# Performance work log

Hardware: AMD Instinct MI355X
Metric: run time of the kernel (lower is better)

The kernel has to match this reference:

```python
import jax, jax.numpy as jnp
import numpy as np

N = 100000   # nodes
E = 3200000  # edges (avg degree 32)
H = 75       # hidden
ITER = 3     # num_layers


def setup_inputs() -> dict:
    key = jax.random.key(0)
    ks = jax.random.split(key, 16)
    s = 0.1  # weight scale
    x = jax.random.normal(ks[0], (N, H), jnp.float32)
    src = jax.random.randint(ks[1], (E,), 0, N)
    dst = jax.random.randint(ks[2], (E,), 0, N)
    edge_index = jnp.stack([src, dst]).astype(jnp.int32)
    rn = lambda k, shp: jax.random.normal(k, shp, jnp.float32) * s
    return {
        "x": x,
        "edge_index": edge_index,
        "eps": jnp.zeros((1,), jnp.float32),      # GIN train_eps, init 0
        "w1": rn(ks[3], (H, H)), "b1": jnp.zeros((H,), jnp.float32),
        "w2": rn(ks[4], (H, H)), "b2": jnp.zeros((H,), jnp.float32),
        "w_ih": rn(ks[5], (3 * H, H)), "w_hh": rn(ks[6], (3 * H, H)),
        "b_ih": jnp.zeros((3 * H,), jnp.float32), "b_hh": jnp.zeros((3 * H,), jnp.float32),
        "wc1": rn(ks[7], (ITER * H, 2 * H)), "bc1": jnp.zeros((2 * H,), jnp.float32),
        "wc2": rn(ks[8], (2 * H, H)), "bc2": jnp.zeros((H,), jnp.float32),
    }


def reference(x, edge_index, eps, w1, b1, w2, b2, w_ih, w_hh, b_ih, b_hh, wc1, bc1, wc2, bc2):
    src, dst = edge_index[0], edge_index[1]

    def gin(xt):
        # sum aggregation over incoming edges (gather -> scatter-add)
        agg = jax.ops.segment_sum(xt[src], dst, num_segments=N)
        z = (1.0 + eps[0]) * xt + agg
        return jnp.maximum(z @ w1 + b1, 0.0) @ w2 + b2

    def gru_step(inp, h):
        # torch.nn.GRU single step; gate order: r, z, n
        gi = inp @ w_ih.T + b_ih
        gh = h @ w_hh.T + b_hh
        ir, iz, inn = jnp.split(gi, 3, axis=-1)
        hr, hz, hn = jnp.split(gh, 3, axis=-1)
        r = jax.nn.sigmoid(ir + hr)
        zg = jax.nn.sigmoid(iz + hz)
        n = jnp.tanh(inn + r * hn)
        return (1.0 - zg) * n + zg * h

    h = x   # h0 = x.unsqueeze(0)
    xt = x
    node_states = []
    for _ in range(ITER):
        m = jnp.maximum(gin(xt), 0.0)
        h = gru_step(m, h)
        xt = h  # GRU output == hidden state for single layer/step
        node_states.append(xt)

    cat = jnp.concatenate(node_states, axis=1)  # [N, ITER*H]
    readout = jnp.maximum(cat @ wc1 + bc1, 0.0) @ wc2 + bc2
    return (xt, readout)
```

## Files before the change

### kernel.cpp

```cpp
#include <hip/hip_runtime.h>

#define NN 100000
#define EE 3200000
#define N2 100032
#define NBUCK 782
#define CPAD 16
#define CHUNK 12288

typedef _Float16 f16;
typedef _Float16 f16x8 __attribute__((ext_vector_type(8)));
typedef float f32x4 __attribute__((ext_vector_type(4)));
typedef unsigned int u32;

#define MFMA(a, b, c) __builtin_amdgcn_mfma_f32_16x16x32_f16((a), (b), (c), 0, 0, 0)


__global__ __launch_bounds__(256) void bhist_kernel(const int4* __restrict__ dst4,
                                                    int* __restrict__ bcnt) {
  __shared__ int h[2][NBUCK];
  int tid = threadIdx.x;
  for (int i = tid; i < 2 * NBUCK; i += 256) ((int*)h)[i] = 0;
  __syncthreads();
  int r = (tid >> 7) & 1;
  for (int i = blockIdx.x * 256 + tid; i < EE / 4; i += gridDim.x * 256) {
    int4 d = dst4[i];
    atomicAdd(&h[r][d.x >> 7], 1);
    atomicAdd(&h[r][d.y >> 7], 1);
    atomicAdd(&h[r][d.z >> 7], 1);
    atomicAdd(&h[r][d.w >> 7], 1);
  }
  __syncthreads();
  for (int i = tid; i < NBUCK; i += 256) {
    int v = h[0][i] + h[1][i];
    if (v) atomicAdd(&bcnt[i * CPAD], v);
  }
}

__global__ __launch_bounds__(1024) void bscan_kernel(const int* __restrict__ bcnt,
                                                     int* __restrict__ bbase,
                                                     int* __restrict__ bcur,
                                                     int* __restrict__ rs) {
  __shared__ int sb[1024];
  int tid = threadIdx.x;
  int c = (tid < NBUCK) ? bcnt[tid * CPAD] : 0;
  int v = c;
  sb[tid] = v;
  __syncthreads();
  for (int off = 1; off < 1024; off <<= 1) {
    int t = (tid >= off) ? sb[tid - off] : 0;
    __syncthreads();
    v += t;
    sb[tid] = v;
    __syncthreads();
  }
  if (tid < NBUCK) {
    bbase[tid] = v - c;
    bcur[tid * CPAD] = v - c;
  }
  if (tid == 0) {
    bbase[NBUCK] = EE;
    rs[NN] = EE;
  }
}

__global__ __launch_bounds__(256) void binB_kernel(const int* __restrict__ src,
                                                   const int* __restrict__ dst,
                                                   int* __restrict__ bcur,
                                                   u32* __restrict__ ebuf) {
  __shared__ int hist[NBUCK];
  __shared__ int base[NBUCK];
  int tid = threadIdx.x;
  int e0 = blockIdx.x * CHUNK;
  int e1 = e0 + CHUNK;
  if (e1 > EE) e1 = EE;
  for (int i = tid; i < NBUCK; i += 256) hist[i] = 0;
  __syncthreads();
  for (int e = e0 + tid * 4; e < e1; e += 1024) {
    int4 d = *(const int4*)(dst + e);
    atomicAdd(&hist[d.x >> 7], 1);
    atomicAdd(&hist[d.y >> 7], 1);
    atomicAdd(&hist[d.z >> 7], 1);
    atomicAdd(&hist[d.w >> 7], 1);
  }
  __syncthreads();
  for (int i = tid; i < NBUCK; i += 256) {
    int c = hist[i];
    if (c) base[i] = atomicAdd(&bcur[i * CPAD], c);
  }
  __syncthreads();
  for (int i = tid; i < NBUCK; i += 256) hist[i] = 0;
  __syncthreads();
  for (int e = e0 + tid * 4; e < e1; e += 1024) {
    int4 d = *(const int4*)(dst + e);
    int4 s = *(const int4*)(src + e);
    int b, loc;
    b = d.x >> 7; loc = atomicAdd(&hist[b], 1);
    ebuf[base[b] + loc] = (u32)s.x | ((u32)(d.x & 127) << 17);
    b = d.y >> 7; loc = atomicAdd(&hist[b], 1);
    ebuf[base[b] + loc] = (u32)s.y | ((u32)(d.y & 127) << 17);
    b = d.z >> 7; loc = atomicAdd(&hist[b], 1);
    ebuf[base[b] + loc] = (u32)s.z | ((u32)(d.z & 127) << 17);
    b = d.w >> 7; loc = atomicAdd(&hist[b], 1);
    ebuf[base[b] + loc] = (u32)s.w | ((u32)(d.w & 127) << 17);
  }
}

__global__ __launch_bounds__(256) void binC_kernel(const u32* __restrict__ ebuf,
                                                   const int* __restrict__ bbase,
                                                   int* __restrict__ rs,
                                                   int* __restrict__ csr) {
  __shared__ int cnt[128], sc[128], cur[128];
  int b = blockIdx.x, tid = threadIdx.x;
  int e0 = bbase[b], e1 = bbase[b + 1];
  if (tid < 128) cnt[tid] = 0;
  __syncthreads();
  for (int e = e0 + tid; e < e1; e += 256) atomicAdd(&cnt[ebuf[e] >> 17], 1);
  __syncthreads();
  if (tid < 128) sc[tid] = cnt[tid];
  __syncthreads();
  for (int off = 1; off < 128; off <<= 1) {
    int t = 0;
    if (tid < 128 && tid >= off) t = sc[tid - off];
    __syncthreads();
    if (tid < 128) sc[tid] += t;
    __syncthreads();
  }
  if (tid < 128) {
    int gpos = e0 + sc[tid] - cnt[tid];
    int node = b * 128 + tid;
    if (node < NN) rs[node] = gpos;
    cur[tid] = gpos;
  }
  __syncthreads();
  for (int e = e0 + tid; e < e1; e += 256) {
    u32 p = ebuf[e];
    int pos = atomicAdd(&cur[p >> 17], 1);
    csr[pos] = (int)(p & 0x1FFFFu);
  }
}


__device__ __forceinline__ f16 pack_one(const float* __restrict__ W,
                                        const float* __restrict__ bias, int rel, int K, int Nc,
                                        int KG, int trans, int bslot) {
  int e = rel & 7, nn = (rel >> 3) & 15;
  int g = (rel >> 7) % KG, nb = (rel >> 7) / KG;
  int k = g * 8 + e, n = nb * 16 + nn;
  float v = 0.f;
  if (n < Nc) {
    if (k < K) v = trans ? W[n * K + k] : W[k * Nc + n];
    else if (k == bslot) v = bias[n];
  }
  return (f16)v;
}

__global__ __launch_bounds__(256) void packall_kernel(const float* __restrict__ w1,
                                                      const float* __restrict__ b1,
                                                      const float* __restrict__ w2,
                                                      const float* __restrict__ b2,
                                                      const float* __restrict__ wih,
                                                      const float* __restrict__ bih,
                                                      const float* __restrict__ whh,
                                                      const float* __restrict__ bhh,
                                                      const float* __restrict__ wc1,
                                                      const float* __restrict__ bc1,
                                                      const float* __restrict__ wc2,
                                                      const float* __restrict__ bc2,
                                                      f16* __restrict__ wp) {
  int i = blockIdx.x * 256 + threadIdx.x;
  if (i >= 120320) return;
  f16 v;
  if (i < 7680) v = pack_one(w1, b1, i, 75, 75, 12, 0, 95);
  else if (i < 15360) v = pack_one(w2, b2, i - 7680, 75, 75, 12, 0, 95);
  else if (i < 38400) {
    int r = i - 15360, g = r / 7680;
    v = pack_one(wih + g * 5625, bih + g * 75, r - g * 7680, 75, 75, 12, 1, 95);
  } else if (i < 61440) {
    int r = i - 38400, g = r / 7680;
    v = pack_one(whh + g * 5625, bhh + g * 75, r - g * 7680, 75, 75, 12, 1, 95);
  } else if (i < 107520) {
    int rel = i - 61440;
    int e = rel & 7, nn = (rel >> 3) & 15;
    int g = (rel >> 7) % 36, nb = (rel >> 7) / 36;
    int q = g * 8 + e, buf = q / 96, kk = q - buf * 96, n = nb * 16 + nn;
    float f = 0.f;
    if (n < 150) {
      if (kk < 75) f = wc1[(buf * 75 + kk) * 150 + n];
      else if (kk == 95 && buf == 0) f = bc1[n];
    }
    v = (f16)f;
  } else v = pack_one(wc2, bc2, i - 107520, 150, 75, 20, 0, 159);
  wp[i] = v;
}


__global__ __launch_bounds__(256) void convx_kernel(const float* __restrict__ x,
                                                    f16* __restrict__ xp) {
  int i = blockIdx.x * 256 + threadIdx.x;
  if (i >= N2 * 96) return;
  int r = i / 96, c = i - r * 96;
  float v = (r < NN && c < 75) ? x[r * 75 + c] : (c == 95 ? 1.f : 0.f);
  xp[i] = (f16)v;
}

__global__ __launch_bounds__(256) void zminit_kernel(f16* __restrict__ zm) {
  int i = blockIdx.x * 256 + threadIdx.x;
  if (i >= N2 * 16) return;
  int r = i >> 4, c = i & 15;
  zm[r * 96 + 80 + c] = (f16)(c == 15 ? 1.f : 0.f);
}


__global__ __launch_bounds__(256) void aggz_kernel(const f16* __restrict__ xc,
                                                   const int* __restrict__ rs,
                                                   const int* __restrict__ csr,
                                                   const float* __restrict__ eps,
                                                   f16* __restrict__ zm) {
  int tid = threadIdx.x;
  int l = tid & 63;
  int n = blockIdx.x * 4 + (tid >> 6);
  if (n >= NN) return;
  int s = l / 10, j = l - s * 10;
  int e0 = rs[n], e1 = rs[n + 1];
  float acc[8] = {0, 0, 0, 0, 0, 0, 0, 0};
  if (l < 60) {
#pragma unroll 2
    for (int e = e0 + s; e < e1; e += 6) {
      int sr = csr[e];
      f16x8 v = *(const f16x8*)(xc + sr * 96 + j * 8);
#pragma unroll
      for (int k = 0; k < 8; ++k) acc[k] += (float)v[k];
    }
  }
  int l1 = (l + 30) & 63, l2 = (l + 10) & 63, l3 = (l + 20) & 63;
#pragma unroll
  for (int k = 0; k < 8; ++k) {
    float t = __shfl(acc[k], l1, 64);
    if (l < 30) acc[k] += t;
    t = __shfl(acc[k], l2, 64);
    if (l < 10) acc[k] += t;
    t = __shfl(acc[k], l3, 64);
    if (l < 10) acc[k] += t;
  }
  if (l < 10) {
    f16x8 self = *(const f16x8*)(xc + n * 96 + j * 8);
    float ep = 1.f + eps[0];
    f16x8 o;
#pragma unroll
    for (int k = 0; k < 8; ++k) o[k] = (f16)(ep * (float)self[k] + acc[k]);
    *(f16x8*)(zm + n * 96 + j * 8) = o;
  }
}


__global__ __launch_bounds__(256) void mlpgru_kernel(const f16* __restrict__ zm,
                                                     const f16* __restrict__ hcur,
                                                     const f16* __restrict__ w1p,
                                                     const f16* __restrict__ w2p,
                                                     const f16* __restrict__ wihp,
                                                     const f16* __restrict__ whhp,
                                                     f16* __restrict__ hb_out,
                                                     float* __restrict__ outx) {
  __shared__ f16 Ls[4][16 * 104];
  __shared__ f16 Hs[4][16 * 104];
  int tid = threadIdx.x;
  int w = tid >> 6, l = tid & 63, lm = l & 15, lg = l >> 4;
  int row0 = blockIdx.x * 64 + w * 16;
  const f16* ar = zm + (row0 + lm) * 96;
  const f16* hr = hcur + (row0 + lm) * 96;
  f16x8 a0 = *(const f16x8*)(ar + lg * 8);
  f16x8 a1 = *(const f16x8*)(ar + 32 + lg * 8);
  f16x8 a2 = *(const f16x8*)(ar + 64 + lg * 8);
  f16x8 h0 = *(const f16x8*)(hr + lg * 8);
  f16x8 h1 = *(const f16x8*)(hr + 32 + lg * 8);
  f16x8 h2 = *(const f16x8*)(hr + 64 + lg * 8);
  f16* Hd = Hs[w];
  *(f16x8*)(Hd + lm * 104 + lg * 8) = h0;
  *(f16x8*)(Hd + lm * 104 + 32 + lg * 8) = h1;
  *(f16x8*)(Hd + lm * 104 + 64 + lg * 8) = h2;
  f32x4 acc[5];
#pragma unroll
  for (int nb = 0; nb < 5; ++nb) {
    acc[nb] = (f32x4){0.f, 0.f, 0.f, 0.f};
    const f16* bp = w1p + ((nb * 12 + lg) * 16 + lm) * 8;
    acc[nb] = MFMA(a0, *(const f16x8*)bp, acc[nb]);
    acc[nb] = MFMA(a1, *(const f16x8*)(bp + 512), acc[nb]);
    acc[nb] = MFMA(a2, *(const f16x8*)(bp + 1024), acc[nb]);
  }
  f16* Ld = Ls[w];
#pragma unroll
  for (int nb = 0; nb < 5; ++nb)
#pragma unroll
    for (int r = 0; r < 4; ++r)
      Ld[(lg * 4 + r) * 104 + nb * 16 + lm] = (f16)fmaxf(acc[nb][r], 0.f);
#pragma unroll
  for (int c = 0; c < 4; ++c) {
    int col = 80 + lg * 4 + c;
    Ld[lm * 104 + col] = (f16)(col == 95 ? 1.f : 0.f);
  }
  const f16* Lr = Ls[w] + lm * 104;
  f16x8 c0 = *(const f16x8*)(Lr + lg * 8);
  f16x8 c1 = *(const f16x8*)(Lr + 32 + lg * 8);
  f16x8 c2 = *(const f16x8*)(Lr + 64 + lg * 8);
  f32x4 acc2[5];
#pragma unroll
  for (int nb = 0; nb < 5; ++nb) {
    acc2[nb] = (f32x4){0.f, 0.f, 0.f, 0.f};
    const f16* bp = w2p + ((nb * 12 + lg) * 16 + lm) * 8;
    acc2[nb] = MFMA(c0, *(const f16x8*)bp, acc2[nb]);
    acc2[nb] = MFMA(c1, *(const f16x8*)(bp + 512), acc2[nb]);
    acc2[nb] = MFMA(c2, *(const f16x8*)(bp + 1024), acc2[nb]);
  }
#pragma unroll
  for (int nb = 0; nb < 5; ++nb)
#pragma unroll
    for (int r = 0; r < 4; ++r)
      Ld[(lg * 4 + r) * 104 + nb * 16 + lm] = (f16)fmaxf(acc2[nb][r], 0.f);
  const f16* mrow = Ls[w] + lm * 104;
  f16x8 am[3];
#pragma unroll
  for (int s = 0; s < 3; ++s) am[s] = *(const f16x8*)(mrow + s * 32 + lg * 8);
  f16x8 ah[3] = {h0, h1, h2};
  f32x4 rg[5], zg[5], ni[5], nh[5];
#pragma unroll
  for (int nb = 0; nb < 5; ++nb) {
    rg[nb] = (f32x4){0.f, 0.f, 0.f, 0.f};
    zg[nb] = rg[nb]; ni[nb] = rg[nb]; nh[nb] = rg[nb];
#pragma unroll
    for (int s = 0; s < 3; ++s) {
      int fo = ((nb * 12 + s * 4 + lg) * 16 + lm) * 8;
      rg[nb] = MFMA(am[s], *(const f16x8*)(wihp + fo), rg[nb]);
      rg[nb] = MFMA(ah[s], *(const f16x8*)(whhp + fo), rg[nb]);
      zg[nb] = MFMA(am[s], *(const f16x8*)(wihp + 7680 + fo), zg[nb]);
      zg[nb] = MFMA(ah[s], *(const f16x8*)(whhp + 7680 + fo), zg[nb]);
      ni[nb] = MFMA(am[s], *(const f16x8*)(wihp + 15360 + fo), ni[nb]);
      nh[nb] = MFMA(ah[s], *(const f16x8*)(whhp + 15360 + fo), nh[nb]);
    }
  }
#pragma unroll
  for (int nb = 0; nb < 5; ++nb)
#pragma unroll
    for (int r = 0; r < 4; ++r) {
      int n = nb * 16 + lm;
      float hval = (float)Hd[(lg * 4 + r) * 104 + n];
      float rv = 1.f / (1.f + __expf(-rg[nb][r]));
      float zv = 1.f / (1.f + __expf(-zg[nb][r]));
      float u = ni[nb][r] + rv * nh[nb][r];
      float t = __expf(-2.f * fabsf(u));
      float nv = copysignf((1.f - t) / (1.f + t), u);
      float hp = zv * (hval - nv) + nv;
      Ld[(lg * 4 + r) * 104 + n] = (f16)hp;
    }
#pragma unroll
  for (int k = 0; k < 3; ++k) {
    int p = l + 64 * k;
    int r = p / 12, sl = p - r * 12;
    f16x8 v = *(const f16x8*)(Ld + r * 104 + sl * 8);
    *(f16x8*)(hb_out + (row0 + r) * 96 + sl * 8) = v;
  }
  if (outx) {
    for (int k = 0; k < 19; ++k) {
      int p = l + 64 * k;
      int gi = row0 * 75 + p;
      if (p < 1200 && gi < NN * 75) {
        int r = p / 75, c = p - r * 75;
        outx[gi] = (float)Ld[r * 104 + c];
      }
    }
  }
}


__global__ __launch_bounds__(256) void readout_kernel(const f16* __restrict__ hb0,
                                                      const f16* __restrict__ hb1,
                                                      const f16* __restrict__ hb2,
                                                      const f16* __restrict__ wc1p,
                                                      const f16* __restrict__ wc2p,
                                                      float* __restrict__ out) {
  __shared__ f16 Ls[4][16 * 168];
  int tid = threadIdx.x;
  int w = tid >> 6, l = tid & 63, lm = l & 15, lg = l >> 4;
  int row0 = blockIdx.x * 64 + w * 16;
  int row = row0 + lm;
  f16x8 a[9];
#pragma unroll
  for (int s = 0; s < 9; ++s) {
    const f16* hb = (s < 3) ? hb0 : (s < 6) ? hb1 : hb2;
    a[s] = *(const f16x8*)(hb + row * 96 + (4 * (s - (s / 3) * 3) + lg) * 8);
  }
  f32x4 acc[10];
#pragma unroll
  for (int nb = 0; nb < 10; ++nb) {
    acc[nb] = (f32x4){0.f, 0.f, 0.f, 0.f};
#pragma unroll
    for (int s = 0; s < 9; ++s)
      acc[nb] = MFMA(a[s], *(const f16x8*)(wc1p + ((nb * 36 + 4 * s + lg) * 16 + lm) * 8),
                     acc[nb]);
  }
  f16* Ld = Ls[w];
#pragma unroll
  for (int nb = 0; nb < 10; ++nb)
#pragma unroll
    for (int r = 0; r < 4; ++r) {
      int n = nb * 16 + lm;
      float v = fmaxf(acc[nb][r], 0.f);
      if (n >= 150) v = (n == 159) ? 1.f : 0.f;
      Ld[(lg * 4 + r) * 168 + n] = (f16)v;
    }
  const f16* Lr = Ls[w] + lm * 168;
  f16x8 a2[5];
#pragma unroll
  for (int s = 0; s < 5; ++s) a2[s] = *(const f16x8*)(Lr + s * 32 + lg * 8);
  f32x4 acc2[5];
#pragma unroll
  for (int nb = 0; nb < 5; ++nb) {
    acc2[nb] = (f32x4){0.f, 0.f, 0.f, 0.f};
#pragma unroll
    for (int s = 0; s < 5; ++s)
      acc2[nb] = MFMA(a2[s], *(const f16x8*)(wc2p + ((nb * 20 + s * 4 + lg) * 16 + lm) * 8),
                     acc2[nb]);
  }
  float* Lf = (float*)Ls[w];
#pragma unroll
  for (int nb = 0; nb < 5; ++nb)
#pragma unroll
    for (int r = 0; r < 4; ++r) {
      int n = nb * 16 + lm;
      if (n < 75) Lf[(lg * 4 + r) * 76 + n] = acc2[nb][r];
    }
  for (int k = 0; k < 19; ++k) {
    int p = l + 64 * k;
    int gi = row0 * 75 + p;
    if (p < 1200 && gi < NN * 75) {
      int r = p / 75, c = p - r * 75;
      out[gi] = Lf[r * 76 + c];
    }
  }
}


extern "C" void kernel_launch(void* const* d_in, const int* in_sizes, int n_in,
                              void* d_out, int out_size, void* d_ws, size_t ws_size,
                              hipStream_t stream) {
  const float* x    = (const float*)d_in[0];
  const int*   ei   = (const int*)d_in[1];
  const float* eps  = (const float*)d_in[2];
  const float* w1   = (const float*)d_in[3];
  const float* b1   = (const float*)d_in[4];
  const float* w2   = (const float*)d_in[5];
  const float* b2   = (const float*)d_in[6];
  const float* w_ih = (const float*)d_in[7];
  const float* w_hh = (const float*)d_in[8];
  const float* b_ih = (const float*)d_in[9];
  const float* b_hh = (const float*)d_in[10];
  const float* wc1  = (const float*)d_in[11];
  const float* bc1  = (const float*)d_in[12];
  const float* wc2  = (const float*)d_in[13];
  const float* bc2  = (const float*)d_in[14];

  const int* srcv = ei;
  const int* dstv = ei + EE;

  float* out_x = (float*)d_out;
  float* out_r = out_x + NN * 75;

  f16* zm   = (f16*)d_ws;
  f16* x0   = zm + (size_t)N2 * 96;
  f16* hb0  = x0 + (size_t)N2 * 96;
  f16* hb1  = hb0 + (size_t)N2 * 96;
  f16* hb2  = hb1 + (size_t)N2 * 96;
  f16* wp   = hb2 + (size_t)N2 * 96;
  f16* w1p  = wp;
  f16* w2p  = wp + 7680;
  f16* wihp = wp + 15360;
  f16* whhp = wp + 38400;
  f16* wc1p = wp + 61440;
  f16* wc2p = wp + 107520;
  u32* ebuf = (u32*)(wp + 120320);
  int* csr  = (int*)(ebuf + EE);
  int* rsv  = csr + EE;
  int* bbase = rsv + NN + 1;
  int* bcur  = bbase + NBUCK + 1;
  int* bcnt  = bcur + NBUCK * CPAD;

  hipMemsetAsync(bcnt, 0, NBUCK * CPAD * sizeof(int), stream);
  bhist_kernel<<<512, 256, 0, stream>>>((const int4*)dstv, bcnt);
  bscan_kernel<<<1, 1024, 0, stream>>>(bcnt, bbase, bcur, rsv);
  binB_kernel<<<(EE + CHUNK - 1) / CHUNK, 256, 0, stream>>>(srcv, dstv, bcur, ebuf);
  binC_kernel<<<NBUCK, 256, 0, stream>>>(ebuf, bbase, rsv, csr);
  convx_kernel<<<(N2 * 96 + 255) / 256, 256, 0, stream>>>(x, x0);
  zminit_kernel<<<(N2 * 16 + 255) / 256, 256, 0, stream>>>(zm);
  packall_kernel<<<470, 256, 0, stream>>>(w1, b1, w2, b2, w_ih, b_ih, w_hh, b_hh,
                                          wc1, bc1, wc2, bc2, wp);

  int gb = N2 / 64;
  f16* hbs[3] = {hb0, hb1, hb2};
  for (int it = 0; it < 3; ++it) {
    const f16* h = (it == 0) ? x0 : hbs[it - 1];
    aggz_kernel<<<25000, 256, 0, stream>>>(h, rsv, csr, eps, zm);
    mlpgru_kernel<<<gb, 256, 0, stream>>>(zm, h, w1p, w2p, wihp, whhp,
                                          hbs[it], (it == 2) ? out_x : nullptr);
  }
  readout_kernel<<<gb, 256, 0, stream>>>(hb0, hb1, hb2, wc1p, wc2p, out_r);
}
```

Before: 667.3 us.

## Merge prep kernels and restructure MFMA loops to cut register pressure

Folds the three setup kernels (weight packing, zm init, x conversion) into one launch indexed by block range, removing two kernel launches. The MLP, GRU and readout kernels now consume each MFMA accumulator right after computing it instead of holding arrays of accumulators, and the GRU gate loop is no longer unrolled, which should lower VGPR use and raise occupancy. The aggregation gather loop unroll goes from 2 to 4 for more memory-level parallelism. The GRU loop being rolled may expose MFMA latency and add loop overhead.

After: 583.0 us. -12.6%, faster.

```diff
diff --git a/kernel.cpp b/kernel.cpp
--- a/kernel.cpp
+++ b/kernel.cpp
@@ -154,60 +154,58 @@
   return (f16)v;
 }
 
-__global__ __launch_bounds__(256) void packall_kernel(const float* __restrict__ w1,
-                                                      const float* __restrict__ b1,
-                                                      const float* __restrict__ w2,
-                                                      const float* __restrict__ b2,
-                                                      const float* __restrict__ wih,
-                                                      const float* __restrict__ bih,
-                                                      const float* __restrict__ whh,
-                                                      const float* __restrict__ bhh,
-                                                      const float* __restrict__ wc1,
-                                                      const float* __restrict__ bc1,
-                                                      const float* __restrict__ wc2,
-                                                      const float* __restrict__ bc2,
-                                                      f16* __restrict__ wp) {
-  int i = blockIdx.x * 256 + threadIdx.x;
-  if (i >= 120320) return;
-  f16 v;
-  if (i < 7680) v = pack_one(w1, b1, i, 75, 75, 12, 0, 95);
-  else if (i < 15360) v = pack_one(w2, b2, i - 7680, 75, 75, 12, 0, 95);
-  else if (i < 38400) {
-    int r = i - 15360, g = r / 7680;
-    v = pack_one(wih + g * 5625, bih + g * 75, r - g * 7680, 75, 75, 12, 1, 95);
-  } else if (i < 61440) {
-    int r = i - 38400, g = r / 7680;
-    v = pack_one(whh + g * 5625, bhh + g * 75, r - g * 7680, 75, 75, 12, 1, 95);
-  } else if (i < 107520) {
-    int rel = i - 61440;
-    int e = rel & 7, nn = (rel >> 3) & 15;
-    int g = (rel >> 7) % 36, nb = (rel >> 7) / 36;
-    int q = g * 8 + e, buf = q / 96, kk = q - buf * 96, n = nb * 16 + nn;
-    float f = 0.f;
-    if (n < 150) {
-      if (kk < 75) f = wc1[(buf * 75 + kk) * 150 + n];
-      else if (kk == 95 && buf == 0) f = bc1[n];
-    }
-    v = (f16)f;
-  } else v = pack_one(wc2, bc2, i - 107520, 150, 75, 20, 0, 159);
-  wp[i] = v;
-}
-
-
-__global__ __launch_bounds__(256) void convx_kernel(const float* __restrict__ x,
-                                                    f16* __restrict__ xp) {
-  int i = blockIdx.x * 256 + threadIdx.x;
-  if (i >= N2 * 96) return;
-  int r = i / 96, c = i - r * 96;
-  float v = (r < NN && c < 75) ? x[r * 75 + c] : (c == 95 ? 1.f : 0.f);
-  xp[i] = (f16)v;
-}
-
-__global__ __launch_bounds__(256) void zminit_kernel(f16* __restrict__ zm) {
-  int i = blockIdx.x * 256 + threadIdx.x;
-  if (i >= N2 * 16) return;
-  int r = i >> 4, c = i & 15;
-  zm[r * 96 + 80 + c] = (f16)(c == 15 ? 1.f : 0.f);
+__global__ __launch_bounds__(256) void prep_kernel(const float* __restrict__ x,
+                                                   f16* __restrict__ xp,
+                                                   f16* __restrict__ zm,
+                                                   const float* __restrict__ w1,
+                                                   const float* __restrict__ b1,
+                                                   const float* __restrict__ w2,
+                                                   const float* __restrict__ b2,
+                                                   const float* __restrict__ wih,
+                                                   const float* __restrict__ bih,
+                                                   const float* __restrict__ whh,
+                                                   const float* __restrict__ bhh,
+                                                   const float* __restrict__ wc1,
+                                                   const float* __restrict__ bc1,
+                                                   const float* __restrict__ wc2,
+                                                   const float* __restrict__ bc2,
+                                                   f16* __restrict__ wp) {
+  int b = blockIdx.x, tid = threadIdx.x;
+  if (b < 470) {
+    int i = b * 256 + tid;
+    if (i >= 120320) return;
+    f16 v;
+    if (i < 7680) v = pack_one(w1, b1, i, 75, 75, 12, 0, 95);
+    else if (i < 15360) v = pack_one(w2, b2, i - 7680, 75, 75, 12, 0, 95);
+    else if (i < 38400) {
+      int r = i - 15360, g = r / 7680;
+      v = pack_one(wih + g * 5625, bih + g * 75, r - g * 7680, 75, 75, 12, 1, 95);
+    } else if (i < 61440) {
+      int r = i - 38400, g = r / 7680;
+      v = pack_one(whh + g * 5625, bhh + g * 75, r - g * 7680, 75, 75, 12, 1, 95);
+    } else if (i < 107520) {
+      int rel = i - 61440;
+      int e = rel & 7, nn = (rel >> 3) & 15;
+      int g = (rel >> 7) % 36, nb = (rel >> 7) / 36;
+      int q = g * 8 + e, buf = q / 96, kk = q - buf * 96, n = nb * 16 + nn;
+      float f = 0.f;
+      if (n < 150) {
+        if (kk < 75) f = wc1[(buf * 75 + kk) * 150 + n];
+        else if (kk == 95 && buf == 0) f = bc1[n];
+      }
+      v = (f16)f;
+    } else v = pack_one(wc2, bc2, i - 107520, 150, 75, 20, 0, 159);
+    wp[i] = v;
+  } else if (b < 6722) {
+    int i = (b - 470) * 256 + tid;
+    int r = i >> 4, c = i & 15;
+    zm[r * 96 + 80 + c] = (f16)(c == 15 ? 1.f : 0.f);
+  } else {
+    int i = (b - 6722) * 256 + tid;
+    int r = i / 96, c = i - r * 96;
+    float v = (r < NN && c < 75) ? x[r * 75 + c] : (c == 95 ? 1.f : 0.f);
+    xp[i] = (f16)v;
+  }
 }
 
 
@@ -224,7 +222,7 @@
   int e0 = rs[n], e1 = rs[n + 1];
   float acc[8] = {0, 0, 0, 0, 0, 0, 0, 0};
   if (l < 60) {
-#pragma unroll 2
+#pragma unroll 4
     for (int e = e0 + s; e < e1; e += 6) {
       int sr = csr[e];
       f16x8 v = *(const f16x8*)(xc + sr * 96 + j * 8);
@@ -278,79 +276,70 @@
   *(f16x8*)(Hd + lm * 104 + lg * 8) = h0;
   *(f16x8*)(Hd + lm * 104 + 32 + lg * 8) = h1;
   *(f16x8*)(Hd + lm * 104 + 64 + lg * 8) = h2;
-  f32x4 acc[5];
+  f16* Ld = Ls[w];
 #pragma unroll
   for (int nb = 0; nb < 5; ++nb) {
-    acc[nb] = (f32x4){0.f, 0.f, 0.f, 0.f};
     const f16* bp = w1p + ((nb * 12 + lg) * 16 + lm) * 8;
-    acc[nb] = MFMA(a0, *(const f16x8*)bp, acc[nb]);
-    acc[nb] = MFMA(a1, *(const f16x8*)(bp + 512), acc[nb]);
-    acc[nb] = MFMA(a2, *(const f16x8*)(bp + 1024), acc[nb]);
-  }
-  f16* Ld = Ls[w];
-#pragma unroll
-  for (int nb = 0; nb < 5; ++nb)
+    f32x4 acc = (f32x4){0.f, 0.f, 0.f, 0.f};
+    acc = MFMA(a0, *(const f16x8*)bp, acc);
+    acc = MFMA(a1, *(const f16x8*)(bp + 512), acc);
+    acc = MFMA(a2, *(const f16x8*)(bp + 1024), acc);
 #pragma unroll
     for (int r = 0; r < 4; ++r)
-      Ld[(lg * 4 + r) * 104 + nb * 16 + lm] = (f16)fmaxf(acc[nb][r], 0.f);
+      Ld[(lg * 4 + r) * 104 + nb * 16 + lm] = (f16)fmaxf(acc[r], 0.f);
+  }
 #pragma unroll
   for (int c = 0; c < 4; ++c) {
     int col = 80 + lg * 4 + c;
     Ld[lm * 104 + col] = (f16)(col == 95 ? 1.f : 0.f);
   }
-  const f16* Lr = Ls[w] + lm * 104;
+  const f16* Lr = Ld + lm * 104;
   f16x8 c0 = *(const f16x8*)(Lr + lg * 8);
   f16x8 c1 = *(const f16x8*)(Lr + 32 + lg * 8);
   f16x8 c2 = *(const f16x8*)(Lr + 64 + lg * 8);
-  f32x4 acc2[5];
 #pragma unroll
   for (int nb = 0; nb < 5; ++nb) {
-    acc2[nb] = (f32x4){0.f, 0.f, 0.f, 0.f};
     const f16* bp = w2p + ((nb * 12 + lg) * 16 + lm) * 8;
-    acc2[nb] = MFMA(c0, *(const f16x8*)bp, acc2[nb]);
-    acc2[nb] = MFMA(c1, *(const f16x8*)(bp + 512), acc2[nb]);
-    acc2[nb] = MFMA(c2, *(const f16x8*)(bp + 1024), acc2[nb]);
-  }
-#pragma unroll
-  for (int nb = 0; nb < 5; ++nb)
+    f32x4 acc = (f32x4){0.f, 0.f, 0.f, 0.f};
+    acc = MFMA(c0, *(const f16x8*)bp, acc);
+    acc = MFMA(c1, *(const f16x8*)(bp + 512), acc);
+    acc = MFMA(c2, *(const f16x8*)(bp + 1024), acc);
 #pragma unroll
     for (int r = 0; r < 4; ++r)
-      Ld[(lg * 4 + r) * 104 + nb * 16 + lm] = (f16)fmaxf(acc2[nb][r], 0.f);
-  const f16* mrow = Ls[w] + lm * 104;
-  f16x8 am[3];
-#pragma unroll
-  for (int s = 0; s < 3; ++s) am[s] = *(const f16x8*)(mrow + s * 32 + lg * 8);
-  f16x8 ah[3] = {h0, h1, h2};
-  f32x4 rg[5], zg[5], ni[5], nh[5];
-#pragma unroll
+      Ld[(lg * 4 + r) * 104 + nb * 16 + lm] = (f16)fmaxf(acc[r], 0.f);
+  }
+  f16x8 am0 = *(const f16x8*)(Lr + lg * 8);
+  f16x8 am1 = *(const f16x8*)(Lr + 32 + lg * 8);
+  f16x8 am2 = *(const f16x8*)(Lr + 64 + lg * 8);
+#pragma unroll 1
   for (int nb = 0; nb < 5; ++nb) {
-    rg[nb] = (f32x4){0.f, 0.f, 0.f, 0.f};
-    zg[nb] = rg[nb]; ni[nb] = rg[nb]; nh[nb] = rg[nb];
+    f32x4 rg = (f32x4){0.f, 0.f, 0.f, 0.f};
+    f32x4 zg = rg, ni = rg, nh = rg;
 #pragma unroll
     for (int s = 0; s < 3; ++s) {
+      f16x8 ams = (s == 0) ? am0 : (s == 1) ? am1 : am2;
+      f16x8 ahs = (s == 0) ? h0 : (s == 1) ? h1 : h2;
       int fo = ((nb * 12 + s * 4 + lg) * 16 + lm) * 8;
-      rg[nb] = MFMA(am[s], *(const f16x8*)(wihp + fo), rg[nb]);
-      rg[nb] = MFMA(ah[s], *(const f16x8*)(whhp + fo), rg[nb]);
-      zg[nb] = MFMA(am[s], *(const f16x8*)(wihp + 7680 + fo), zg[nb]);
-      zg[nb] = MFMA(ah[s], *(const f16x8*)(whhp + 7680 + fo), zg[nb]);
-      ni[nb] = MFMA(am[s], *(const f16x8*)(wihp + 15360 + fo), ni[nb]);
-      nh[nb] = MFMA(ah[s], *(const f16x8*)(whhp + 15360 + fo), nh[nb]);
-    }
-  }
-#pragma unroll
-  for (int nb = 0; nb < 5; ++nb)
+      rg = MFMA(ams, *(const f16x8*)(wihp + fo), rg);
+      rg = MFMA(ahs, *(const f16x8*)(whhp + fo), rg);
+      zg = MFMA(ams, *(const f16x8*)(wihp + 7680 + fo), zg);
+      zg = MFMA(ahs, *(const f16x8*)(whhp + 7680 + fo), zg);
+      ni = MFMA(ams, *(const f16x8*)(wihp + 15360 + fo), ni);
+      nh = MFMA(ahs, *(const f16x8*)(whhp + 15360 + fo), nh);
+    }
 #pragma unroll
     for (int r = 0; r < 4; ++r) {
       int n = nb * 16 + lm;
       float hval = (float)Hd[(lg * 4 + r) * 104 + n];
-      float rv = 1.f / (1.f + __expf(-rg[nb][r]));
-      float zv = 1.f / (1.f + __expf(-zg[nb][r]));
-      float u = ni[nb][r] + rv * nh[nb][r];
+      float rv = 1.f / (1.f + __expf(-rg[r]));
+      float zv = 1.f / (1.f + __expf(-zg[r]));
+      float u = ni[r] + rv * nh[r];
       float t = __expf(-2.f * fabsf(u));
       float nv = copysignf((1.f - t) / (1.f + t), u);
       float hp = zv * (hval - nv) + nv;
       Ld[(lg * 4 + r) * 104 + n] = (f16)hp;
     }
+  }
 #pragma unroll
   for (int k = 0; k < 3; ++k) {
     int p = l + 64 * k;
@@ -388,25 +377,21 @@
     const f16* hb = (s < 3) ? hb0 : (s < 6) ? hb1 : hb2;
     a[s] = *(const f16x8*)(hb + row * 96 + (4 * (s - (s / 3) * 3) + lg) * 8);
   }
-  f32x4 acc[10];
+  f16* Ld = Ls[w];
 #pragma unroll
   for (int nb = 0; nb < 10; ++nb) {
-    acc[nb] = (f32x4){0.f, 0.f, 0.f, 0.f};
+    f32x4 acc = (f32x4){0.f, 0.f, 0.f, 0.f};
 #pragma unroll
     for (int s = 0; s < 9; ++s)
-      acc[nb] = MFMA(a[s], *(const f16x8*)(wc1p + ((nb * 36 + 4 * s + lg) * 16 + lm) * 8),
-                     acc[nb]);
-  }
-  f16* Ld = Ls[w];
-#pragma unroll
-  for (int nb = 0; nb < 10; ++nb)
+      acc = MFMA(a[s], *(const f16x8*)(wc1p + ((nb * 36 + 4 * s + lg) * 16 + lm) * 8), acc);
 #pragma unroll
     for (int r = 0; r < 4; ++r) {
       int n = nb * 16 + lm;
-      float v = fmaxf(acc[nb][r], 0.f);
+      float v = fmaxf(acc[r], 0.f);
       if (n >= 150) v = (n == 159) ? 1.f : 0.f;
       Ld[(lg * 4 + r) * 168 + n] = (f16)v;
     }
+  }
   const f16* Lr = Ls[w] + lm * 168;
   f16x8 a2[5];
 #pragma unroll
@@ -418,7 +403,7 @@
 #pragma unroll
     for (int s = 0; s < 5; ++s)
       acc2[nb] = MFMA(a2[s], *(const f16x8*)(wc2p + ((nb * 20 + s * 4 + lg) * 16 + lm) * 8),
-                     acc2[nb]);
+                      acc2[nb]);
   }
   float* Lf = (float*)Ls[w];
 #pragma unroll
@@ -488,10 +473,8 @@
   bscan_kernel<<<1, 1024, 0, stream>>>(bcnt, bbase, bcur, rsv);
   binB_kernel<<<(EE + CHUNK - 1) / CHUNK, 256, 0, stream>>>(srcv, dstv, bcur, ebuf);
   binC_kernel<<<NBUCK, 256, 0, stream>>>(ebuf, bbase, rsv, csr);
-  convx_kernel<<<(N2 * 96 + 255) / 256, 256, 0, stream>>>(x, x0);
-  zminit_kernel<<<(N2 * 16 + 255) / 256, 256, 0, stream>>>(zm);
-  packall_kernel<<<470, 256, 0, stream>>>(w1, b1, w2, b2, w_ih, b_ih, w_hh, b_hh,
-                                          wc1, bc1, wc2, bc2, wp);
+  prep_kernel<<<44234, 256, 0, stream>>>(x, x0, zm, w1, b1, w2, b2, w_ih, b_ih,
+                                         w_hh, b_hh, wc1, bc1, wc2, bc2, wp);
 
   int gb = N2 / 64;
   f16* hbs[3] = {hb0, hb1, hb2};
```
